# Optimization experiments

Measured on AMD Instinct MI355X. Metric: run time of the kernel, lower is better.

Reference implementation:

```python
import jax, jax.numpy as jnp
import numpy as np


def setup_inputs() -> dict:
    key = jax.random.key(0)
    k1, k2, k3, k4 = jax.random.split(key, 4)
    B, Cin, H, W = 16, 64, 96, 96
    D, O, KH, KW, S = 100, 256, 3, 3, 3
    x = jax.random.normal(k1, (B, Cin, H, W), dtype=jnp.float32)
    dictionary = jax.random.normal(k2, (D, Cin, KH, KW), dtype=jnp.float32) * 0.05
    lookup_coefficients = jax.random.normal(k3, (O, KH, KW, S), dtype=jnp.float32) * 0.1
    lookup_indices = jax.random.randint(k4, (O, KH, KW, S), 0, D, dtype=jnp.int64)
    return {
        "x": x,
        "dictionary": dictionary,
        "lookup_coefficients": lookup_coefficients,
        "lookup_indices": lookup_indices,
    }


def reference(x, dictionary, lookup_coefficients, lookup_indices):
    # Dense conv with the small dictionary: [B, Cin, H, W] x [D, Cin, kh, kw] -> [B, D, Oh, Ow]
    conv_out = jax.lax.conv_general_dilated(
        x, dictionary,
        window_strides=(1, 1),
        padding=((1, 1), (1, 1)),
        dimension_numbers=("NCHW", "OIHW", "NCHW"),
    )
    O = lookup_coefficients.shape[0]
    D = dictionary.shape[0]
    # Flatten kernel-position and sparsity axes: each (position, slot) contributes
    # coeff * conv_out[:, idx] to output channel o; COO duplicates sum.
    idx = lookup_indices.reshape(O, -1)      # [O, P*S]
    coeff = lookup_coefficients.reshape(O, -1)  # [O, P*S]
    # Scatter-add into a per-output-channel weight over dictionary entries: W[o, d]
    Wmat = jnp.zeros((O, D), dtype=conv_out.dtype).at[jnp.arange(O)[:, None], idx].add(coeff)
    # Gather-weighted-sum == sparse (O x D) matmul against conv_out channels
    out = jnp.einsum("od,bdhw->bohw", Wmat, conv_out)
    return out
```

## Files before the change

kernel.cpp:

```cpp
#include <hip/hip_runtime.h>

#define NB   16
#define CIN  64
#define HH   96
#define WW   96
#define DD   100
#define OO   256
#define NWG  (NB * HH)
#define NCV  (NB * HH * 2)
#define WPAD 50

typedef __attribute__((ext_vector_type(8))) short  bf16x8;
typedef __attribute__((ext_vector_type(4))) float  f32x4;

#define FSWZ(wp) ((((wp) ^ ((wp) >> 3)) & 7) << 4)

static __device__ __forceinline__ unsigned short f32_to_bf16(float f) {
    unsigned int u = __float_as_uint(f);
    u += 0x7FFFu + ((u >> 16) & 1u);
    return (unsigned short)(u >> 16);
}

__global__ __launch_bounds__(256) void prep_kernel(
    const float* __restrict__ x, const float* __restrict__ dict,
    const float* __restrict__ coeff, const int* __restrict__ idx,
    unsigned short* __restrict__ x2, unsigned short* __restrict__ weff2,
    unsigned short* __restrict__ zbuf)
{
    __shared__ unsigned short lds[CIN * 100];
    __shared__ float wrow[DD];
    const int blk = blockIdx.x, tid = threadIdx.x;

    if (blk < NWG) {
        const int b = blk / HH, h = blk % HH;
        for (int it = 0; it < 6; ++it) {
            int i = tid + it * 256;
            int c = i / 24, w4 = i % 24;
            float4 v = *reinterpret_cast<const float4*>(
                x + (((size_t)(b * CIN + c) * HH + h) * WW + w4 * 4));
            ushort4 u;
            u.x = f32_to_bf16(v.x); u.y = f32_to_bf16(v.y);
            u.z = f32_to_bf16(v.z); u.w = f32_to_bf16(v.w);
            *reinterpret_cast<ushort4*>(&lds[c * 100 + w4 * 4]) = u;
        }
        __syncthreads();
        for (int it = 0; it < 6; ++it) {
            int i = tid + it * 256;
            int w = i / 16, c = (i % 16) * 4;
            ushort4 u;
            u.x = lds[(c + 0) * 100 + w];
            u.y = lds[(c + 1) * 100 + w];
            u.z = lds[(c + 2) * 100 + w];
            u.w = lds[(c + 3) * 100 + w];
            *reinterpret_cast<ushort4*>(x2 + (((size_t)(b * HH + h) * WW + w) * CIN + c)) = u;
        }
    } else {
        const int o = blk - NWG;
        if (o == 0 && tid < 8) zbuf[tid] = 0;
        if (tid < DD) wrow[tid] = 0.f;
        __syncthreads();
        if (tid == 0) {
            for (int s = 0; s < 27; ++s) wrow[idx[o * 27 + s]] += coeff[o * 27 + s];
        }
        __syncthreads();
        for (int j = tid; j < 576; j += 256) {
            int kpos = j >> 6, c = j & 63;
            float s = 0.f;
            for (int d = 0; d < DD; ++d)
                s += wrow[d] * dict[d * 576 + c * 9 + kpos];
            int otile = o >> 4, ks = c >> 5;
            int lane8 = (o & 15) | (((c >> 3) & 3) << 4);
            weff2[((size_t)(kpos * 32 + otile * 2 + ks)) * 512 + lane8 * 8 + (c & 7)]
                = f32_to_bf16(s);
        }
    }
}

__global__ __launch_bounds__(256, 3) void conv_kernel(
    const unsigned short* __restrict__ x2,
    const unsigned short* __restrict__ weff2,
    const unsigned short* __restrict__ zbuf,
    float* __restrict__ out)
{
    __shared__ unsigned short xs[3 * WPAD * 64];

    const int wg  = blockIdx.x;
    const int swz = (wg & 7) * (NCV / 8) + (wg >> 3);
    const int b = swz / 192, rem = swz % 192;
    const int h = rem >> 1, ws = (rem & 1) * 48;
    const int tid = threadIdx.x;
    const int lane = tid & 63, wn = tid >> 6;
    const int l15 = lane & 15;

    char* xsb = reinterpret_cast<char*>(xs);
    const char* x2b = reinterpret_cast<const char*>(x2) + (size_t)b * HH * WW * 128;
    const char* zbp = reinterpret_cast<const char*>(zbuf);

    const unsigned short* wbase = weff2 + (size_t)(wn * 8) * 512 + lane * 8;
    bf16x8 bfr[4][4];
#pragma unroll
    for (int s = 0; s < 4; ++s)
#pragma unroll
        for (int n = 0; n < 4; ++n)
            bfr[s][n] = *reinterpret_cast<const bf16x8*>(
                wbase + (((s >> 1) * 32) + n * 2 + (s & 1)) * 512);

#pragma unroll
    for (int it = 0; it < 5; ++it) {
        int chunk = tid + it * 256;
        if (chunk < 1200) {
            int r = chunk / 400, rem2 = chunk % 400;
            int wp = rem2 >> 3, gb = (rem2 & 7) << 4;
            int hp = h - 1 + r, w = ws - 1 + wp;
            const char* src = (w >= 0 && w < WW && hp >= 0 && hp < HH)
                ? x2b + ((size_t)(hp * WW + w) * 128 + (gb ^ FSWZ(wp)))
                : zbp;
            __builtin_amdgcn_global_load_lds(
                (const __attribute__((address_space(1))) void*)src,
                (__attribute__((address_space(3))) void*)(xsb + chunk * 16),
                16, 0, 0);
        }
    }

    f32x4 acc[3][4];
#pragma unroll
    for (int m = 0; m < 3; ++m)
#pragma unroll
        for (int n = 0; n < 4; ++n)
            acc[m][n] = (f32x4){0.f, 0.f, 0.f, 0.f};

    __syncthreads();

    bf16x8 ax[2][3];
    {
        const int cb0 = ((lane >> 4) * 8) * 2;
#pragma unroll
        for (int m = 0; m < 3; ++m) {
            int wpos = m * 16 + l15;
            ax[0][m] = *reinterpret_cast<const bf16x8*>(
                xsb + wpos * 128 + (cb0 ^ FSWZ(wpos)));
        }
    }

#pragma unroll
    for (int s = 0; s < 18; ++s) {
        if (s < 17) {
            const int s1 = s + 1;
            const int kpos1 = s1 >> 1, ks1 = s1 & 1;
            const int kh1 = kpos1 / 3, dw1 = kpos1 % 3;
            const int cb1 = (ks1 * 32 + (lane >> 4) * 8) * 2;
#pragma unroll
            for (int m = 0; m < 3; ++m) {
                int wpos = m * 16 + l15 + dw1;
                ax[s1 & 1][m] = *reinterpret_cast<const bf16x8*>(
                    xsb + kh1 * 6400 + wpos * 128 + (cb1 ^ FSWZ(wpos)));
            }
        }
        __builtin_amdgcn_s_setprio(1);
#pragma unroll
        for (int m = 0; m < 3; ++m)
#pragma unroll
            for (int n = 0; n < 4; ++n)
                acc[m][n] = __builtin_amdgcn_mfma_f32_16x16x32_bf16(
                    ax[s & 1][m], bfr[s & 3][n], acc[m][n], 0, 0, 0);
        __builtin_amdgcn_s_setprio(0);
        if (s < 14) {
            const int s4 = s + 4;
            const int off = (s4 >> 1) * 32 + (s4 & 1);
#pragma unroll
            for (int n = 0; n < 4; ++n)
                bfr[s & 3][n] = *reinterpret_cast<const bf16x8*>(
                    wbase + (off + n * 2) * 512);
        }
    }

#pragma unroll
    for (int m = 0; m < 3; ++m)
#pragma unroll
        for (int n = 0; n < 4; ++n) {
            int o = wn * 64 + n * 16 + l15;
            int w = ws + m * 16 + (lane >> 4) * 4;
            *reinterpret_cast<f32x4*>(
                out + (((size_t)(b * OO + o) * HH + h) * WW + w)) = acc[m][n];
        }
}

extern "C" void kernel_launch(void* const* d_in, const int* in_sizes, int n_in,
                              void* d_out, int out_size, void* d_ws, size_t ws_size,
                              hipStream_t stream) {
    const float* x     = (const float*)d_in[0];
    const float* dict  = (const float*)d_in[1];
    const float* coeff = (const float*)d_in[2];
    const int*   idx   = (const int*)d_in[3];
    float* out = (float*)d_out;

    char* ws = (char*)d_ws;
    unsigned short* weff2 = (unsigned short*)ws;
    unsigned short* zbuf  = (unsigned short*)(ws + 294912);
    unsigned short* x2    = (unsigned short*)(ws + 1048576);

    prep_kernel<<<NWG + OO, 256, 0, stream>>>(x, dict, coeff, idx, x2, weff2, zbuf);
    conv_kernel<<<NCV, 256, 0, stream>>>(x2, weff2, zbuf, out);
}
```

Baseline: 79.54 us.

## Retile conv into two output rows by half of output channels per workgroup

Each conv workgroup now computes two adjacent output rows for half of the 256 output channels, where before it computed one row for all channels. It stages four input rows in LDS instead of three, so each staged row is reused across both output rows. Each wave holds half as many weight fragments and reuses them across both rows. The grid size stays at 3072. Per-workgroup input staging rises from 3 to 4 rows, and each input tile is now loaded by two workgroups (one per channel half), which may offset the reuse gain.

```diff
diff --git a/kernel.cpp b/kernel.cpp
--- a/kernel.cpp
+++ b/kernel.cpp
@@ -7,7 +7,7 @@
 #define DD   100
 #define OO   256
 #define NWG  (NB * HH)
-#define NCV  (NB * HH * 2)
+#define NCV  3072
 #define WPAD 50
 
 typedef __attribute__((ext_vector_type(8))) short  bf16x8;
@@ -82,12 +82,13 @@
     const unsigned short* __restrict__ zbuf,
     float* __restrict__ out)
 {
-    __shared__ unsigned short xs[3 * WPAD * 64];
+    __shared__ unsigned short xs[4 * WPAD * 64];
 
     const int wg  = blockIdx.x;
     const int swz = (wg & 7) * (NCV / 8) + (wg >> 3);
     const int b = swz / 192, rem = swz % 192;
-    const int h = rem >> 1, ws = (rem & 1) * 48;
+    const int hp = rem >> 2, wh = (rem >> 1) & 1, oh = rem & 1;
+    const int h0 = hp * 2, ws = wh * 48;
     const int tid = threadIdx.x;
     const int lane = tid & 63, wn = tid >> 6;
     const int l15 = lane & 15;
@@ -96,24 +97,25 @@
     const char* x2b = reinterpret_cast<const char*>(x2) + (size_t)b * HH * WW * 128;
     const char* zbp = reinterpret_cast<const char*>(zbuf);
 
-    const unsigned short* wbase = weff2 + (size_t)(wn * 8) * 512 + lane * 8;
-    bf16x8 bfr[4][4];
-#pragma unroll
-    for (int s = 0; s < 4; ++s)
-#pragma unroll
-        for (int n = 0; n < 4; ++n)
-            bfr[s][n] = *reinterpret_cast<const bf16x8*>(
-                wbase + (((s >> 1) * 32) + n * 2 + (s & 1)) * 512);
-
-#pragma unroll
-    for (int it = 0; it < 5; ++it) {
+    const unsigned short* wbase = weff2 + (size_t)((oh * 8 + wn * 2) * 2) * 512 + lane * 8;
+    bf16x8 bfr[4][2];
+#pragma unroll
+    for (int s = 0; s < 4; ++s) {
+        const int off = (s >> 1) * 32 + (s & 1);
+#pragma unroll
+        for (int n = 0; n < 2; ++n)
+            bfr[s][n] = *reinterpret_cast<const bf16x8*>(wbase + (off + n * 2) * 512);
+    }
+
+#pragma unroll
+    for (int it = 0; it < 7; ++it) {
         int chunk = tid + it * 256;
-        if (chunk < 1200) {
+        if (chunk < 1600) {
             int r = chunk / 400, rem2 = chunk % 400;
             int wp = rem2 >> 3, gb = (rem2 & 7) << 4;
-            int hp = h - 1 + r, w = ws - 1 + wp;
-            const char* src = (w >= 0 && w < WW && hp >= 0 && hp < HH)
-                ? x2b + ((size_t)(hp * WW + w) * 128 + (gb ^ FSWZ(wp)))
+            int hx = h0 - 1 + r, w = ws - 1 + wp;
+            const char* src = (w >= 0 && w < WW && hx >= 0 && hx < HH)
+                ? x2b + ((size_t)(hx * WW + w) * 128 + (gb ^ FSWZ(wp)))
                 : zbp;
             __builtin_amdgcn_global_load_lds(
                 (const __attribute__((address_space(1))) void*)src,
@@ -122,24 +124,28 @@
         }
     }
 
-    f32x4 acc[3][4];
-#pragma unroll
-    for (int m = 0; m < 3; ++m)
-#pragma unroll
-        for (int n = 0; n < 4; ++n)
-            acc[m][n] = (f32x4){0.f, 0.f, 0.f, 0.f};
+    f32x4 acc[2][3][2];
+#pragma unroll
+    for (int q = 0; q < 2; ++q)
+#pragma unroll
+        for (int m = 0; m < 3; ++m)
+#pragma unroll
+            for (int n = 0; n < 2; ++n)
+                acc[q][m][n] = (f32x4){0.f, 0.f, 0.f, 0.f};
 
     __syncthreads();
 
-    bf16x8 ax[2][3];
+    bf16x8 ax[2][2][3];
     {
         const int cb0 = ((lane >> 4) * 8) * 2;
 #pragma unroll
-        for (int m = 0; m < 3; ++m) {
-            int wpos = m * 16 + l15;
-            ax[0][m] = *reinterpret_cast<const bf16x8*>(
-                xsb + wpos * 128 + (cb0 ^ FSWZ(wpos)));
-        }
+        for (int q = 0; q < 2; ++q)
+#pragma unroll
+            for (int m = 0; m < 3; ++m) {
+                int wpos = m * 16 + l15;
+                ax[0][q][m] = *reinterpret_cast<const bf16x8*>(
+                    xsb + q * 6400 + wpos * 128 + (cb0 ^ FSWZ(wpos)));
+            }
     }
 
 #pragma unroll
@@ -150,39 +156,46 @@
             const int kh1 = kpos1 / 3, dw1 = kpos1 % 3;
             const int cb1 = (ks1 * 32 + (lane >> 4) * 8) * 2;
 #pragma unroll
-            for (int m = 0; m < 3; ++m) {
-                int wpos = m * 16 + l15 + dw1;
-                ax[s1 & 1][m] = *reinterpret_cast<const bf16x8*>(
-                    xsb + kh1 * 6400 + wpos * 128 + (cb1 ^ FSWZ(wpos)));
-            }
+            for (int q = 0; q < 2; ++q)
+#pragma unroll
+                for (int m = 0; m < 3; ++m) {
+                    int wpos = m * 16 + l15 + dw1;
+                    ax[s1 & 1][q][m] = *reinterpret_cast<const bf16x8*>(
+                        xsb + (kh1 + q) * 6400 + wpos * 128 + (cb1 ^ FSWZ(wpos)));
+                }
         }
         __builtin_amdgcn_s_setprio(1);
 #pragma unroll
-        for (int m = 0; m < 3; ++m)
-#pragma unroll
-            for (int n = 0; n < 4; ++n)
-                acc[m][n] = __builtin_amdgcn_mfma_f32_16x16x32_bf16(
-                    ax[s & 1][m], bfr[s & 3][n], acc[m][n], 0, 0, 0);
+        for (int q = 0; q < 2; ++q)
+#pragma unroll
+            for (int m = 0; m < 3; ++m)
+#pragma unroll
+                for (int n = 0; n < 2; ++n)
+                    acc[q][m][n] = __builtin_amdgcn_mfma_f32_16x16x32_bf16(
+                        ax[s & 1][q][m], bfr[s & 3][n], acc[q][m][n], 0, 0, 0);
         __builtin_amdgcn_s_setprio(0);
         if (s < 14) {
             const int s4 = s + 4;
             const int off = (s4 >> 1) * 32 + (s4 & 1);
 #pragma unroll
-            for (int n = 0; n < 4; ++n)
+            for (int n = 0; n < 2; ++n)
                 bfr[s & 3][n] = *reinterpret_cast<const bf16x8*>(
                     wbase + (off + n * 2) * 512);
         }
     }
 
 #pragma unroll
-    for (int m = 0; m < 3; ++m)
-#pragma unroll
-        for (int n = 0; n < 4; ++n) {
-            int o = wn * 64 + n * 16 + l15;
-            int w = ws + m * 16 + (lane >> 4) * 4;
-            *reinterpret_cast<f32x4*>(
-                out + (((size_t)(b * OO + o) * HH + h) * WW + w)) = acc[m][n];
-        }
+    for (int q = 0; q < 2; ++q)
+#pragma unroll
+        for (int m = 0; m < 3; ++m)
+#pragma unroll
+            for (int n = 0; n < 2; ++n) {
+                int o = oh * 128 + wn * 32 + n * 16 + l15;
+                int w = ws + m * 16 + (lane >> 4) * 4;
+                *reinterpret_cast<f32x4*>(
+                    out + (((size_t)(b * OO + o) * HH + h0 + q) * WW + w))
+                    = acc[q][m][n];
+            }
 }
 
 extern "C" void kernel_launch(void* const* d_in, const int* in_sizes, int n_in,
```

New measurement: 69.52 us. 1.14x faster.
